# Performance work log

Measured on AMD Instinct MI355X. Metric: run time of the kernel, lower is better.

Reference implementation:

```python
import jax, jax.numpy as jnp
import numpy as np

POOL_H, POOL_W = 7, 7


def _crop_and_resize_one(feat, boxes, pool_h, pool_w):
    """TF crop_and_resize-style bilinear sampling.
    feat: [H, W, C]; boxes: [N, 4] normalized (y1, x1, y2, x2).
    Returns [N, pool_h, pool_w, C].
    """
    H, W, C = feat.shape
    y1, x1, y2, x2 = boxes[:, 0], boxes[:, 1], boxes[:, 2], boxes[:, 3]
    fy = jnp.arange(pool_h, dtype=feat.dtype) / (pool_h - 1)  # [ph] in [0,1]
    fx = jnp.arange(pool_w, dtype=feat.dtype) / (pool_w - 1)  # [pw]
    ys = (y1[:, None] + fy[None, :] * (y2 - y1)[:, None]) * (H - 1)  # [N, ph]
    xs = (x1[:, None] + fx[None, :] * (x2 - x1)[:, None]) * (W - 1)  # [N, pw]
    y0f = jnp.clip(jnp.floor(ys), 0, H - 1)
    x0f = jnp.clip(jnp.floor(xs), 0, W - 1)
    y0 = y0f.astype(jnp.int32)
    x0 = x0f.astype(jnp.int32)
    y1i = jnp.clip(y0 + 1, 0, H - 1)
    x1i = jnp.clip(x0 + 1, 0, W - 1)
    wy = (ys - y0f)[:, :, None, None]  # [N, ph, 1, 1]
    wx = (xs - x0f)[:, None, :, None]  # [N, 1, pw, 1]
    # four corner gathers -> [N, ph, pw, C]
    f00 = feat[y0[:, :, None], x0[:, None, :]]
    f01 = feat[y0[:, :, None], x1i[:, None, :]]
    f10 = feat[y1i[:, :, None], x0[:, None, :]]
    f11 = feat[y1i[:, :, None], x1i[:, None, :]]
    top = f00 + (f01 - f00) * wx
    bot = f10 + (f11 - f10) * wx
    return top + (bot - top) * wy


def setup_inputs() -> dict:
    key = jax.random.key(0)
    kf, kb = jax.random.split(key)
    B, H, W, C, N = 2, 64, 64, 256, 2000
    features = jax.random.normal(kf, (B, H, W, C), dtype=jnp.float32)
    p = jax.random.uniform(kb, (B, N, 4), dtype=jnp.float32)
    # ensure valid normalized boxes (y1<=y2, x1<=x2)
    rois = jnp.stack([
        jnp.minimum(p[..., 0], p[..., 2]),
        jnp.minimum(p[..., 1], p[..., 3]),
        jnp.maximum(p[..., 0], p[..., 2]),
        jnp.maximum(p[..., 1], p[..., 3]),
    ], axis=-1)
    return {"features": features, "rois": rois}


def reference(features, rois):
    # [B, N, 7, 7, C]
    return jax.vmap(lambda f, b: _crop_and_resize_one(f, b, POOL_H, POOL_W))(features, rois)
```

## Files before the change

### kernel.cpp

```cpp
#include <hip/hip_runtime.h>


#define POOL 7

__global__ __launch_bounds__(256) void roialign_kernel(
    const float* __restrict__ feat,
    const float* __restrict__ rois,
    float* __restrict__ out,
    int B, int H, int W, int C, int N)
{
    const int lane = threadIdx.x & 63;
    const int wid  = threadIdx.x >> 6;
    const long long w = (long long)blockIdx.x * 4 + wid;
    const long long total = (long long)B * N * POOL * POOL;
    if (w >= total) return;

    const int pp = (int)(w % (POOL * POOL));
    const long long bn = w / (POOL * POOL);
    const int px = pp % POOL;
    const int py = pp / POOL;
    const int n  = (int)(bn % N);
    const int b  = (int)(bn / N);

    const float* r = rois + ((long long)b * N + n) * 4;
    const float ry1 = r[0], rx1 = r[1], ry2 = r[2], rx2 = r[3];

    const float fy = (float)py / (float)(POOL - 1);
    const float fx = (float)px / (float)(POOL - 1);
    const float ys = (ry1 + fy * (ry2 - ry1)) * (float)(H - 1);
    const float xs = (rx1 + fx * (rx2 - rx1)) * (float)(W - 1);

    const float y0f = fminf(fmaxf(floorf(ys), 0.0f), (float)(H - 1));
    const float x0f = fminf(fmaxf(floorf(xs), 0.0f), (float)(W - 1));
    const int y0 = (int)y0f;
    const int x0 = (int)x0f;
    const int y1i = min(y0 + 1, H - 1);
    const int x1i = min(x0 + 1, W - 1);
    const float wy = ys - y0f;
    const float wx = xs - x0f;

    const int C4 = C >> 2;
    const float4* fb = (const float4*)(feat + (long long)b * H * W * C);

    const long long i00 = ((long long)y0  * W + x0 ) * C4 + lane;
    const long long i01 = ((long long)y0  * W + x1i) * C4 + lane;
    const long long i10 = ((long long)y1i * W + x0 ) * C4 + lane;
    const long long i11 = ((long long)y1i * W + x1i) * C4 + lane;

    const float4 f00 = fb[i00];
    const float4 f01 = fb[i01];
    const float4 f10 = fb[i10];
    const float4 f11 = fb[i11];

    float4 o;
    {
        float tx, bx;
        tx = f00.x + (f01.x - f00.x) * wx;
        bx = f10.x + (f11.x - f10.x) * wx;
        o.x = tx + (bx - tx) * wy;
        tx = f00.y + (f01.y - f00.y) * wx;
        bx = f10.y + (f11.y - f10.y) * wx;
        o.y = tx + (bx - tx) * wy;
        tx = f00.z + (f01.z - f00.z) * wx;
        bx = f10.z + (f11.z - f10.z) * wx;
        o.z = tx + (bx - tx) * wy;
        tx = f00.w + (f01.w - f00.w) * wx;
        bx = f10.w + (f11.w - f10.w) * wx;
        o.w = tx + (bx - tx) * wy;
    }

    ((float4*)out)[w * C4 + lane] = o;
}

extern "C" void kernel_launch(void* const* d_in, const int* in_sizes, int n_in,
                              void* d_out, int out_size, void* d_ws, size_t ws_size,
                              hipStream_t stream) {
    const int B = 2, H = 64, W = 64, C = 256;
    const int N = in_sizes[1] / (B * 4);

    const float* feat = (const float*)d_in[0];
    const float* rois = (const float*)d_in[1];
    float* out = (float*)d_out;

    const long long total_pixels = (long long)B * N * POOL * POOL;
    const int waves_per_block = 4;
    const int blocks = (int)((total_pixels + waves_per_block - 1) / waves_per_block);

    roialign_kernel<<<blocks, 256, 0, stream>>>(feat, rois, out, B, H, W, C, N);
}
```

Before: 234.4 us.

## Process a full pooled row per wave and map batches to XCD groups

Each wave now computes one output row of seven pixels, sharing the ROI load and y-interpolation setup and issuing 28 independent float4 loads in an unrolled loop. Block indices are remapped so each batch's feature map goes to half of the eight XCDs, keeping that batch's 4 MB feature map in the L2 of those XCDs. This trades more per-wave work and higher register pressure for fewer blocks, better memory-level parallelism and better cache locality.

```diff
diff --git a/kernel.cpp b/kernel.cpp
--- a/kernel.cpp
+++ b/kernel.cpp
@@ -7,53 +7,58 @@
     const float* __restrict__ feat,
     const float* __restrict__ rois,
     float* __restrict__ out,
-    int B, int H, int W, int C, int N)
+    int H, int W, int C4, int N, int blocks_per_batch)
 {
     const int lane = threadIdx.x & 63;
     const int wid  = threadIdx.x >> 6;
-    const long long w = (long long)blockIdx.x * 4 + wid;
-    const long long total = (long long)B * N * POOL * POOL;
-    if (w >= total) return;
 
-    const int pp = (int)(w % (POOL * POOL));
-    const long long bn = w / (POOL * POOL);
-    const int px = pp % POOL;
-    const int py = pp / POOL;
-    const int n  = (int)(bn % N);
-    const int b  = (int)(bn / N);
+    const int xcd  = blockIdx.x & 7;
+    const int slot = blockIdx.x >> 3;
+    const int b    = xcd >> 2;
+    const int lblock = slot * 4 + (xcd & 3);
+    if (lblock >= blocks_per_batch) return;
+
+    const int row = lblock * 4 + wid;
+    const int rows_per_batch = N * POOL;
+    if (row >= rows_per_batch) return;
+
+    const int n  = row / POOL;
+    const int py = row - n * POOL;
 
     const float* r = rois + ((long long)b * N + n) * 4;
     const float ry1 = r[0], rx1 = r[1], ry2 = r[2], rx2 = r[3];
 
-    const float fy = (float)py / (float)(POOL - 1);
-    const float fx = (float)px / (float)(POOL - 1);
+    const float fy = (float)py * (1.0f / (POOL - 1));
     const float ys = (ry1 + fy * (ry2 - ry1)) * (float)(H - 1);
-    const float xs = (rx1 + fx * (rx2 - rx1)) * (float)(W - 1);
+    const float y0f = fminf(fmaxf(floorf(ys), 0.0f), (float)(H - 1));
+    const int   y0  = (int)y0f;
+    const int   y1i = min(y0 + 1, H - 1);
+    const float wy  = ys - y0f;
 
-    const float y0f = fminf(fmaxf(floorf(ys), 0.0f), (float)(H - 1));
-    const float x0f = fminf(fmaxf(floorf(xs), 0.0f), (float)(W - 1));
-    const int y0 = (int)y0f;
-    const int x0 = (int)x0f;
-    const int y1i = min(y0 + 1, H - 1);
-    const int x1i = min(x0 + 1, W - 1);
-    const float wy = ys - y0f;
-    const float wx = xs - x0f;
+    const float4* fb = (const float4*)feat + (long long)b * H * W * C4;
+    const float4* r0 = fb + (long long)y0  * W * C4;
+    const float4* r1 = fb + (long long)y1i * W * C4;
 
-    const int C4 = C >> 2;
-    const float4* fb = (const float4*)(feat + (long long)b * H * W * C);
+    float4* ob = (float4*)out +
+                 (((long long)b * N + n) * (POOL * POOL) + (long long)py * POOL) * C4 + lane;
 
-    const long long i00 = ((long long)y0  * W + x0 ) * C4 + lane;
-    const long long i01 = ((long long)y0  * W + x1i) * C4 + lane;
-    const long long i10 = ((long long)y1i * W + x0 ) * C4 + lane;
-    const long long i11 = ((long long)y1i * W + x1i) * C4 + lane;
+    const float dx = rx2 - rx1;
 
-    const float4 f00 = fb[i00];
-    const float4 f01 = fb[i01];
-    const float4 f10 = fb[i10];
-    const float4 f11 = fb[i11];
+#pragma unroll
+    for (int px = 0; px < POOL; ++px) {
+        const float fx  = (float)px * (1.0f / (POOL - 1));
+        const float xs  = (rx1 + fx * dx) * (float)(W - 1);
+        const float x0f = fminf(fmaxf(floorf(xs), 0.0f), (float)(W - 1));
+        const int   x0  = (int)x0f;
+        const int   x1i = min(x0 + 1, W - 1);
+        const float wx  = xs - x0f;
 
-    float4 o;
-    {
+        const float4 f00 = r0[x0  * C4 + lane];
+        const float4 f01 = r0[x1i * C4 + lane];
+        const float4 f10 = r1[x0  * C4 + lane];
+        const float4 f11 = r1[x1i * C4 + lane];
+
+        float4 o;
         float tx, bx;
         tx = f00.x + (f01.x - f00.x) * wx;
         bx = f10.x + (f11.x - f10.x) * wx;
@@ -67,9 +72,9 @@
         tx = f00.w + (f01.w - f00.w) * wx;
         bx = f10.w + (f11.w - f10.w) * wx;
         o.w = tx + (bx - tx) * wy;
+
+        ob[px * C4] = o;
     }
-
-    ((float4*)out)[w * C4 + lane] = o;
 }
 
 extern "C" void kernel_launch(void* const* d_in, const int* in_sizes, int n_in,
@@ -82,9 +87,11 @@
     const float* rois = (const float*)d_in[1];
     float* out = (float*)d_out;
 
-    const long long total_pixels = (long long)B * N * POOL * POOL;
-    const int waves_per_block = 4;
-    const int blocks = (int)((total_pixels + waves_per_block - 1) / waves_per_block);
+    const int rows_per_batch   = N * POOL;
+    const int blocks_per_batch = (rows_per_batch + 3) / 4;
+    const int slots  = (blocks_per_batch + 3) / 4;
+    const int blocks = slots * 8;
 
-    roialign_kernel<<<blocks, 256, 0, stream>>>(feat, rois, out, B, H, W, C, N);
+    roialign_kernel<<<blocks, 256, 0, stream>>>(feat, rois, out,
+                                                H, W, C / 4, N, blocks_per_batch);
 }
```

New measurement: 218.1 us. -7.0%, faster.
